# Kernel optimization log

Hardware: AMD Instinct MI355X
Metric: run time of the kernel (lower is better)

Reference implementation:

```python
import jax, jax.numpy as jnp
import numpy as np

PC_RANGE = np.array([-20.0, -20.0, -2.3, 20.0, 20.0, 0.9], np.float32)
GRID = np.array([0.1, 0.1, 0.1], np.float32)
K = 5                      # kernel_size
C_IN, C_OUT = 128, 128
BS, G = 8, 2000
SPATIAL = tuple(int(s) for s in ((PC_RANGE[3:] - PC_RANGE[:3]) / GRID).astype(np.int32))  # (400,400,32)


def setup_inputs() -> dict:
    key = jax.random.key(0)
    k1, k2, k3 = jax.random.split(key, 3)
    instance_feature = jax.random.normal(k1, (BS, G, C_IN), jnp.float32)
    anchor = jax.random.uniform(k2, (BS, G, 3), jnp.float32)          # normalized xyz in [0,1)
    w = jax.random.normal(k3, (K ** 3, C_IN, C_OUT), jnp.float32) * 0.02  # SubMConv3d weight, flattened offsets
    return {"instance_feature": instance_feature, "anchor": anchor, "w": w}


def _voxel_indices(anchor):
    # cartesian(): map normalized anchor xyz into the pc_range box, then voxelize.
    lo = jnp.asarray(PC_RANGE[:3])
    hi = jnp.asarray(PC_RANGE[3:])
    xyz = anchor[..., :3] * (hi - lo) + lo                 # [bs, g, 3]
    idx = ((xyz - lo) / jnp.asarray(GRID)).astype(jnp.int32)
    return idx


def reference(instance_feature, anchor, w):
    bs, g, c = instance_feature.shape
    n = bs * g
    idx = _voxel_indices(anchor).reshape(n, 3)             # [n, 3] int32 voxel coords
    bidx = jnp.repeat(jnp.arange(bs, dtype=jnp.int32), g)  # [n]
    Dx, Dy, Dz = SPATIAL

    # Rulebook substitute: dense voxel -> point-id lookup (-1 = inactive).
    grid = jnp.full((bs, Dx, Dy, Dz), -1, jnp.int32)
    grid = grid.at[bidx, idx[:, 0], idx[:, 1], idx[:, 2]].set(jnp.arange(n, dtype=jnp.int32))

    feats = instance_feature.reshape(n, c)
    r = (K - 1) // 2
    ax = jnp.arange(-r, r + 1, dtype=jnp.int32)
    offs = jnp.stack(jnp.meshgrid(ax, ax, ax, indexing="ij"), -1).reshape(-1, 3)  # [K^3, 3]
    dims = jnp.asarray([Dx, Dy, Dz], jnp.int32)

    # Submanifold conv: gather neighbor features per kernel offset, matmul, accumulate.
    def step(acc, inp):
        off, wk = inp                                       # off [3], wk [Cin, Cout]
        nb = idx + off[None, :]                             # [n, 3]
        inb = jnp.all((nb >= 0) & (nb < dims[None, :]), axis=-1)
        nbc = jnp.clip(nb, 0, dims[None, :] - 1)
        j = grid[bidx, nbc[:, 0], nbc[:, 1], nbc[:, 2]]     # [n] neighbor point id or -1
        valid = inb & (j >= 0)
        fj = jnp.where(valid[:, None], feats[jnp.clip(j, 0, n - 1)], 0.0)  # [n, Cin]
        return acc + fj @ wk, None

    out0 = jnp.zeros((n, C_OUT), feats.dtype)
    out, _ = jax.lax.scan(step, out0, (offs, w))
    return out.reshape(bs, g, C_OUT)                        # output_proj = Identity
```

## Files before the change

### kernel.cpp

```cpp
#include <hip/hip_runtime.h>
#include <stdint.h>

#define BSZ 8
#define GQ 2000
#define NPTS (BSZ * GQ)
#define CH 128
#define HCAP 8
#define TM 16
#define NTHR 256
#define AS_LD 129
#define KB 32
#define ZPAD 32
#define EMPTY16 0xAAAAu


__device__ __forceinline__ int3 voxel_idx(const float* __restrict__ anchor, int i,
                                          float sx, float sy, float sz,
                                          float lx, float ly, float lz, float g) {
    float ax = anchor[i * 3 + 0];
    float ay = anchor[i * 3 + 1];
    float az = anchor[i * 3 + 2];
    float x = __fadd_rn(__fmul_rn(ax, sx), lx);
    float y = __fadd_rn(__fmul_rn(ay, sy), ly);
    float z = __fadd_rn(__fmul_rn(az, sz), lz);
    int ix = (int)__fdiv_rn(__fsub_rn(x, lx), g);
    int iy = (int)__fdiv_rn(__fsub_rn(y, ly), g);
    int iz = (int)__fdiv_rn(__fsub_rn(z, lz), g);
    return make_int3(ix, iy, iz);
}

__global__ void build_grid_kernel(const float* __restrict__ anchor,
                                  unsigned int* __restrict__ grid32,
                                  float sx, float sy, float sz,
                                  float lx, float ly, float lz, float g,
                                  int Dx, int Dy, int Dz) {
    int i = blockIdx.x * blockDim.x + threadIdx.x;
    if (i >= NPTS) return;
    int3 v = voxel_idx(anchor, i, sx, sy, sz, lx, ly, lz, g);
    if (v.x < 0 || v.x >= Dx || v.y < 0 || v.y >= Dy || v.z < 0 || v.z >= Dz) return;
    int b = i / GQ;
    size_t cell = ((size_t)(b * Dx + v.x) * Dy + v.y) * ZPAD + v.z;
    unsigned int* wp = grid32 + (cell >> 1);
    int sh = (int)(cell & 1) * 16;
    unsigned int old = *wp;
    for (;;) {
        unsigned int cur = (old >> sh) & 0xFFFFu;
        unsigned int nj = (cur == EMPTY16) ? (unsigned int)i
                          : (cur > (unsigned int)i ? cur : (unsigned int)i);
        unsigned int neu = (old & ~(0xFFFFu << sh)) | (nj << sh);
        unsigned int got = atomicCAS(wp, old, neu);
        if (got == old) break;
        old = got;
    }
}

__global__ void __launch_bounds__(NTHR)
fused_kernel(const float* __restrict__ feat,
             const float* __restrict__ anchor,
             const float* __restrict__ w,
             const unsigned short* __restrict__ grid16,
             float* __restrict__ out,
             float sx, float sy, float sz,
             float lx, float ly, float lz, float g,
             int Dx, int Dy, int Dz) {
    __shared__ float As[TM * AS_LD];
    __shared__ float Bs[KB * CH];
    __shared__ int4  vox[TM];
    __shared__ int   selfj[TM];
    __shared__ int   s_hn[TM];
    __shared__ int   s_hits[TM * HCAP];

    int rowbase = blockIdx.x * TM;
    int t = threadIdx.x;

    if (t < TM) {
        int i = rowbase + t;
        int3 v = voxel_idx(anchor, i, sx, sy, sz, lx, ly, lz, g);
        vox[t] = make_int4(v.x, v.y, v.z, i / GQ);
        selfj[t] = -1;
        s_hn[t] = 0;
    }
    __syncthreads();

    for (int f = t; f < TM * 25; f += NTHR) {
        int p = f / 25;
        int col = f - p * 25;
        int4 v = vox[p];
        int ox = col / 5 - 2;
        int oy = col - (col / 5) * 5 - 2;
        int nx = v.x + ox, ny = v.y + oy;
        if (nx < 0 || nx >= Dx || ny < 0 || ny >= Dy) continue;
        int zlo = v.z - 2; if (zlo < 0) zlo = 0;
        int zhi = v.z + 2; if (zhi > Dz - 1) zhi = Dz - 1;
        if (zlo > zhi) continue;
        int g0 = zlo >> 2;
        int g1 = g0 + 1; if (g1 > (ZPAD / 4 - 1)) g1 = ZPAD / 4 - 1;
        size_t colbase = ((size_t)(v.w * Dx + nx) * Dy + ny) * ZPAD;
        ushort4 q0 = *(const ushort4*)(grid16 + colbase + g0 * 4);
        ushort4 q1 = *(const ushort4*)(grid16 + colbase + g1 * 4);
        unsigned short e0 = q0.x, e1 = q0.y, e2 = q0.z, e3 = q0.w;
        unsigned short e4 = q1.x, e5 = q1.y, e6 = q1.z, e7 = q1.w;
        unsigned short ee[8] = {e0, e1, e2, e3, e4, e5, e6, e7};
        int zbase = g0 * 4;
        #pragma unroll
        for (int c = 0; c < 8; ++c) {
            int z4 = zbase + c;
            if (z4 < zlo || z4 > zhi) continue;
            int j = ee[c];
            if (j >= NPTS) continue;
            int oz = z4 - v.z;
            int koff = (ox + 2) * 25 + (oy + 2) * 5 + (oz + 2);
            if (koff == 62) {
                selfj[p] = j;
            } else {
                int pos = atomicAdd(&s_hn[p], 1);
                if (pos < HCAP) s_hits[p * HCAP + pos] = (koff << 14) | j;
            }
        }
    }
    __syncthreads();

    #pragma unroll
    for (int f = t; f < TM * 32; f += NTHR) {
        int r = f >> 5;
        int c4 = f & 31;
        int j = selfj[r];
        float4 val = make_float4(0.f, 0.f, 0.f, 0.f);
        if (j >= 0) val = *(const float4*)(feat + (size_t)j * CH + c4 * 4);
        float* dst = As + r * AS_LD + c4 * 4;
        dst[0] = val.x; dst[1] = val.y; dst[2] = val.z; dst[3] = val.w;
    }

    int tc = t & 31;
    int tr = t >> 5;
    int r0 = tr * 2;

    float acc[2][4];
    #pragma unroll
    for (int a = 0; a < 2; ++a)
        #pragma unroll
        for (int b = 0; b < 4; ++b) acc[a][b] = 0.f;

    const float* B = w + (size_t)62 * CH * CH;

    #pragma unroll
    for (int chunk = 0; chunk < CH / KB; ++chunk) {
        __syncthreads();
        #pragma unroll
        for (int f = t; f < KB * 32; f += NTHR) {
            int kk = f >> 5;
            int c4 = f & 31;
            *(float4*)(Bs + kk * CH + c4 * 4) =
                *(const float4*)(B + (size_t)(chunk * KB + kk) * CH + c4 * 4);
        }
        __syncthreads();

        #pragma unroll 4
        for (int kk = 0; kk < KB; ++kk) {
            float4 b4 = *(const float4*)(Bs + kk * CH + tc * 4);
            float a0 = As[(r0 + 0) * AS_LD + chunk * KB + kk];
            float a1 = As[(r0 + 1) * AS_LD + chunk * KB + kk];
            acc[0][0] = fmaf(a0, b4.x, acc[0][0]); acc[0][1] = fmaf(a0, b4.y, acc[0][1]);
            acc[0][2] = fmaf(a0, b4.z, acc[0][2]); acc[0][3] = fmaf(a0, b4.w, acc[0][3]);
            acc[1][0] = fmaf(a1, b4.x, acc[1][0]); acc[1][1] = fmaf(a1, b4.y, acc[1][1]);
            acc[1][2] = fmaf(a1, b4.z, acc[1][2]); acc[1][3] = fmaf(a1, b4.w, acc[1][3]);
        }
    }

    #pragma unroll
    for (int rr = 0; rr < 2; ++rr) {
        int r = r0 + rr;
        int nh = s_hn[r];
        if (nh > HCAP) nh = HCAP;
        for (int h = 0; h < nh; ++h) {
            int packed = s_hits[r * HCAP + h];
            int k = packed >> 14;
            int j = packed & 0x3FFF;
            const float* fj = feat + (size_t)j * CH;
            const float* wk = w + (size_t)k * CH * CH + tc * 4;
            #pragma unroll 8
            for (int c = 0; c < CH; ++c) {
                float a = fj[c];
                float4 b4 = *(const float4*)(wk + (size_t)c * CH);
                acc[rr][0] = fmaf(a, b4.x, acc[rr][0]);
                acc[rr][1] = fmaf(a, b4.y, acc[rr][1]);
                acc[rr][2] = fmaf(a, b4.z, acc[rr][2]);
                acc[rr][3] = fmaf(a, b4.w, acc[rr][3]);
            }
        }
        int i = rowbase + r;
        float4 v = make_float4(acc[rr][0], acc[rr][1], acc[rr][2], acc[rr][3]);
        *(float4*)(out + (size_t)i * CH + tc * 4) = v;
    }
}

extern "C" void kernel_launch(void* const* d_in, const int* in_sizes, int n_in,
                              void* d_out, int out_size, void* d_ws, size_t ws_size,
                              hipStream_t stream) {
    const float* feat   = (const float*)d_in[0];
    const float* anchor = (const float*)d_in[1];
    const float* w      = (const float*)d_in[2];
    float* out = (float*)d_out;

    unsigned int*   grid32 = (unsigned int*)d_ws;
    unsigned short* grid16 = (unsigned short*)d_ws;

    float lx = -20.0f, ly = -20.0f, lz = -2.3f;
    float hx =  20.0f, hy =  20.0f, hz =  0.9f;
    float sx = hx - lx, sy = hy - ly, sz = hz - lz;
    float g = 0.1f;
    int Dx = (int)(sx / g);
    int Dy = (int)(sy / g);
    int Dz = (int)(sz / g);

    build_grid_kernel<<<(NPTS + 255) / 256, 256, 0, stream>>>(
        anchor, grid32, sx, sy, sz, lx, ly, lz, g, Dx, Dy, Dz);

    fused_kernel<<<NPTS / TM, NTHR, 0, stream>>>(
        feat, anchor, w, grid16, out, sx, sy, sz, lx, ly, lz, g, Dx, Dy, Dz);
}
```

Before: 101.5 us.

## Move sparse neighbor contributions into a separate atomic scatter kernel

The fused kernel no longer processes neighbor hits inline. Those hits used to serialize a few warps per block over per-row loops that read weights from global memory. Each block now compacts its non-self neighbor hits into a global list, and a third kernel then processes one hit per block and atomically adds the product into the output. This aims to stop the rare neighbor work from stalling whole blocks, at the cost of an extra launch, float atomics (non-deterministic summation order), and a fixed hit capacity that could silently drop contributions.

```diff
diff --git a/kernel.cpp b/kernel.cpp
--- a/kernel.cpp
+++ b/kernel.cpp
@@ -5,14 +5,17 @@
 #define GQ 2000
 #define NPTS (BSZ * GQ)
 #define CH 128
-#define HCAP 8
 #define TM 16
 #define NTHR 256
 #define AS_LD 129
 #define KB 32
 #define ZPAD 32
 #define EMPTY16 0xAAAAu
-
+#define BHCAP 64
+#define HIT_CAP 8192
+
+#define GCNT_OFF  83886080
+#define GHITS_OFF (GCNT_OFF + 256)
 
 __device__ __forceinline__ int3 voxel_idx(const float* __restrict__ anchor, int i,
                                           float sx, float sy, float sz,
@@ -31,10 +34,12 @@
 
 __global__ void build_grid_kernel(const float* __restrict__ anchor,
                                   unsigned int* __restrict__ grid32,
+                                  int* __restrict__ gcnt,
                                   float sx, float sy, float sz,
                                   float lx, float ly, float lz, float g,
                                   int Dx, int Dy, int Dz) {
     int i = blockIdx.x * blockDim.x + threadIdx.x;
+    if (i == 0) gcnt[0] = 0;
     if (i >= NPTS) return;
     int3 v = voxel_idx(anchor, i, sx, sy, sz, lx, ly, lz, g);
     if (v.x < 0 || v.x >= Dx || v.y < 0 || v.y >= Dy || v.z < 0 || v.z >= Dz) return;
@@ -59,6 +64,8 @@
              const float* __restrict__ anchor,
              const float* __restrict__ w,
              const unsigned short* __restrict__ grid16,
+             int* __restrict__ gcnt,
+             int2* __restrict__ ghits,
              float* __restrict__ out,
              float sx, float sy, float sz,
              float lx, float ly, float lz, float g,
@@ -67,45 +74,53 @@
     __shared__ float Bs[KB * CH];
     __shared__ int4  vox[TM];
     __shared__ int   selfj[TM];
-    __shared__ int   s_hn[TM];
-    __shared__ int   s_hits[TM * HCAP];
+    __shared__ int   s_cnt;
+    __shared__ int   s_base;
+    __shared__ int   s_hits[BHCAP];
 
     int rowbase = blockIdx.x * TM;
     int t = threadIdx.x;
 
+    if (t == 0) { s_cnt = 0; s_base = 0; }
     if (t < TM) {
         int i = rowbase + t;
         int3 v = voxel_idx(anchor, i, sx, sy, sz, lx, ly, lz, g);
         vox[t] = make_int4(v.x, v.y, v.z, i / GQ);
         selfj[t] = -1;
-        s_hn[t] = 0;
     }
     __syncthreads();
 
-    for (int f = t; f < TM * 25; f += NTHR) {
-        int p = f / 25;
+    #pragma unroll
+    for (int it = 0; it < 2; ++it) {
+        int f = t + it * NTHR;
+        bool tvalid = f < TM * 25;
+        int p = tvalid ? f / 25 : 0;
         int col = f - p * 25;
         int4 v = vox[p];
         int ox = col / 5 - 2;
         int oy = col - (col / 5) * 5 - 2;
         int nx = v.x + ox, ny = v.y + oy;
-        if (nx < 0 || nx >= Dx || ny < 0 || ny >= Dy) continue;
         int zlo = v.z - 2; if (zlo < 0) zlo = 0;
         int zhi = v.z + 2; if (zhi > Dz - 1) zhi = Dz - 1;
-        if (zlo > zhi) continue;
-        int g0 = zlo >> 2;
-        int g1 = g0 + 1; if (g1 > (ZPAD / 4 - 1)) g1 = ZPAD / 4 - 1;
-        size_t colbase = ((size_t)(v.w * Dx + nx) * Dy + ny) * ZPAD;
-        ushort4 q0 = *(const ushort4*)(grid16 + colbase + g0 * 4);
-        ushort4 q1 = *(const ushort4*)(grid16 + colbase + g1 * 4);
-        unsigned short e0 = q0.x, e1 = q0.y, e2 = q0.z, e3 = q0.w;
-        unsigned short e4 = q1.x, e5 = q1.y, e6 = q1.z, e7 = q1.w;
-        unsigned short ee[8] = {e0, e1, e2, e3, e4, e5, e6, e7};
-        int zbase = g0 * 4;
+        bool colok = tvalid && nx >= 0 && nx < Dx && ny >= 0 && ny < Dy && zlo <= zhi;
+        unsigned short ee[8];
+        int zbase = (zlo >> 2) * 4;
+        if (colok) {
+            int g0 = zlo >> 2;
+            int g1 = g0 + 1; if (g1 > (ZPAD / 4 - 1)) g1 = ZPAD / 4 - 1;
+            size_t colbase = ((size_t)(v.w * Dx + nx) * Dy + ny) * ZPAD;
+            ushort4 q0 = *(const ushort4*)(grid16 + colbase + g0 * 4);
+            ushort4 q1 = *(const ushort4*)(grid16 + colbase + g1 * 4);
+            ee[0] = q0.x; ee[1] = q0.y; ee[2] = q0.z; ee[3] = q0.w;
+            ee[4] = q1.x; ee[5] = q1.y; ee[6] = q1.z; ee[7] = q1.w;
+        } else {
+            #pragma unroll
+            for (int c = 0; c < 8; ++c) ee[c] = 0xFFFF;
+        }
         #pragma unroll
         for (int c = 0; c < 8; ++c) {
             int z4 = zbase + c;
-            if (z4 < zlo || z4 > zhi) continue;
+            if (!colok || z4 < zlo || z4 > zhi) continue;
             int j = ee[c];
             if (j >= NPTS) continue;
             int oz = z4 - v.z;
@@ -113,12 +128,24 @@
             if (koff == 62) {
                 selfj[p] = j;
             } else {
-                int pos = atomicAdd(&s_hn[p], 1);
-                if (pos < HCAP) s_hits[p * HCAP + pos] = (koff << 14) | j;
+                int pos = atomicAdd(&s_cnt, 1);
+                if (pos < BHCAP) s_hits[pos] = (p << 21) | (koff << 14) | j;
             }
         }
     }
     __syncthreads();
+
+    int nh = s_cnt < BHCAP ? s_cnt : BHCAP;
+    if (t == 0 && nh > 0) s_base = atomicAdd(gcnt, nh);
+    __syncthreads();
+    if (t < nh) {
+        int e = s_hits[t];
+        int p = e >> 21;
+        int pos = s_base + t;
+        if (pos < HIT_CAP)
+            ghits[pos] = make_int2(((rowbase + p) << 7) | ((e >> 14) & 0x7F),
+                                   e & 0x3FFF);
+    }
 
     #pragma unroll
     for (int f = t; f < TM * 32; f += NTHR) {
@@ -169,28 +196,40 @@
 
     #pragma unroll
     for (int rr = 0; rr < 2; ++rr) {
-        int r = r0 + rr;
-        int nh = s_hn[r];
-        if (nh > HCAP) nh = HCAP;
-        for (int h = 0; h < nh; ++h) {
-            int packed = s_hits[r * HCAP + h];
-            int k = packed >> 14;
-            int j = packed & 0x3FFF;
-            const float* fj = feat + (size_t)j * CH;
-            const float* wk = w + (size_t)k * CH * CH + tc * 4;
-            #pragma unroll 8
-            for (int c = 0; c < CH; ++c) {
-                float a = fj[c];
-                float4 b4 = *(const float4*)(wk + (size_t)c * CH);
-                acc[rr][0] = fmaf(a, b4.x, acc[rr][0]);
-                acc[rr][1] = fmaf(a, b4.y, acc[rr][1]);
-                acc[rr][2] = fmaf(a, b4.z, acc[rr][2]);
-                acc[rr][3] = fmaf(a, b4.w, acc[rr][3]);
-            }
-        }
-        int i = rowbase + r;
+        int i = rowbase + r0 + rr;
         float4 v = make_float4(acc[rr][0], acc[rr][1], acc[rr][2], acc[rr][3]);
         *(float4*)(out + (size_t)i * CH + tc * 4) = v;
+    }
+}
+
+__global__ void __launch_bounds__(CH)
+scatter_kernel(const float* __restrict__ feat,
+               const float* __restrict__ w,
+               const int2* __restrict__ ghits,
+               const int* __restrict__ gcnt,
+               float* __restrict__ out) {
+    __shared__ float fbuf[CH];
+    int n = gcnt[0];
+    if (n > HIT_CAP) n = HIT_CAP;
+    int t = threadIdx.x;
+    for (int h = blockIdx.x; h < n; h += gridDim.x) {
+        int2 e = ghits[h];
+        int i = e.x >> 7;
+        int k = e.x & 0x7F;
+        int j = e.y;
+        __syncthreads();
+        fbuf[t] = feat[(size_t)j * CH + t];
+        __syncthreads();
+        const float* wk = w + (size_t)k * CH * CH + t;
+        float a0 = 0.f, a1 = 0.f, a2 = 0.f, a3 = 0.f;
+        #pragma unroll 16
+        for (int c = 0; c < CH; c += 4) {
+            a0 = fmaf(fbuf[c + 0], wk[(c + 0) * CH], a0);
+            a1 = fmaf(fbuf[c + 1], wk[(c + 1) * CH], a1);
+            a2 = fmaf(fbuf[c + 2], wk[(c + 2) * CH], a2);
+            a3 = fmaf(fbuf[c + 3], wk[(c + 3) * CH], a3);
+        }
+        atomicAdd(&out[(size_t)i * CH + t], (a0 + a1) + (a2 + a3));
     }
 }
 
@@ -202,8 +241,11 @@
     const float* w      = (const float*)d_in[2];
     float* out = (float*)d_out;
 
-    unsigned int*   grid32 = (unsigned int*)d_ws;
-    unsigned short* grid16 = (unsigned short*)d_ws;
+    char* ws = (char*)d_ws;
+    unsigned int*   grid32 = (unsigned int*)ws;
+    unsigned short* grid16 = (unsigned short*)ws;
+    int*  gcnt  = (int*)(ws + GCNT_OFF);
+    int2* ghits = (int2*)(ws + GHITS_OFF);
 
     float lx = -20.0f, ly = -20.0f, lz = -2.3f;
     float hx =  20.0f, hy =  20.0f, hz =  0.9f;
@@ -214,8 +256,11 @@
     int Dz = (int)(sz / g);
 
     build_grid_kernel<<<(NPTS + 255) / 256, 256, 0, stream>>>(
-        anchor, grid32, sx, sy, sz, lx, ly, lz, g, Dx, Dy, Dz);
+        anchor, grid32, gcnt, sx, sy, sz, lx, ly, lz, g, Dx, Dy, Dz);
 
     fused_kernel<<<NPTS / TM, NTHR, 0, stream>>>(
-        feat, anchor, w, grid16, out, sx, sy, sz, lx, ly, lz, g, Dx, Dy, Dz);
-}
+        feat, anchor, w, grid16, gcnt, ghits, out,
+        sx, sy, sz, lx, ly, lz, g, Dx, Dy, Dz);
+
+    scatter_kernel<<<2048, CH, 0, stream>>>(feat, w, ghits, gcnt, out);
+}
```

Measured after the change: 99.11 us. -2.4%, faster.
